# Performance work log

Hardware: AMD Instinct MI355X
Metric: run time of the kernel (lower is better)

The kernel has to match this reference:

```python
import jax, jax.numpy as jnp
import numpy as np

SOC, EOS = 3, 2
NUM_HEADS = 12
LN_EPS = 1e-5


def setup_inputs() -> dict:
    key = jax.random.key(0)
    ks = jax.random.split(key, 24)
    B, S, D, N, FF, K = 8, 4096, 768, 1024, 3072, 640
    img = jax.random.normal(ks[0], (B, N, D), jnp.float32)
    hid = jax.random.normal(ks[1], (B, S, D), jnp.float32)
    seq = jax.random.randint(ks[2], (B, S), 4, 100)
    m = jax.random.uniform(ks[3], (B, S)) < 0.125
    seq = jnp.where(m, SOC, seq).at[:, 0].set(SOC)  # ensure >=1 SOC per row
    w = lambda k, a, b: jax.random.normal(k, (a, b), jnp.float32) * 0.02
    return {
        "img": img, "hid": hid, "seq": seq,
        "wq_s": w(ks[4], D, D), "wk_s": w(ks[5], D, D), "wv_s": w(ks[6], D, D), "wo_s": w(ks[7], D, D),
        "wq_c": w(ks[8], D, D), "wk_c": w(ks[9], D, D), "wv_c": w(ks[10], D, D), "wo_c": w(ks[11], D, D),
        "w_ff1": w(ks[12], D, FF), "w_ff2": w(ks[13], FF, D),
        "ln1_s": jnp.ones((D,)), "ln1_b": jnp.zeros((D,)),
        "ln2_s": jnp.ones((D,)), "ln2_b": jnp.zeros((D,)),
        "ln3_s": jnp.ones((D,)), "ln3_b": jnp.zeros((D,)),
        "cap": K,
    }


def _ln(x, s, b):
    mu = jnp.mean(x, axis=-1, keepdims=True)
    var = jnp.var(x, axis=-1, keepdims=True)
    return (x - mu) * jax.lax.rsqrt(var + LN_EPS) * s + b


def _mha(q_in, kv_in, wq, wk, wv, wo, key_mask):
    # q_in [B,Lq,D], kv_in [B,Lk,D], key_mask [B,Lk] bool or None
    B, Lq, D = q_in.shape
    H = NUM_HEADS
    dh = D // H
    q = (q_in @ wq).reshape(B, Lq, H, dh)
    k = (kv_in @ wk).reshape(B, -1, H, dh)
    v = (kv_in @ wv).reshape(B, -1, H, dh)
    scores = jnp.einsum("bqhd,bkhd->bhqk", q, k) / np.sqrt(dh).astype(q.dtype)
    if key_mask is not None:
        scores = jnp.where(key_mask[:, None, None, :], scores, jnp.asarray(-1e9, scores.dtype))
    att = jax.nn.softmax(scores, axis=-1)
    out = jnp.einsum("bhqk,bkhd->bqhd", att, v).reshape(B, Lq, D)
    return out @ wo


def _extract(data, mask, cap):
    # data [B,S,...], mask [B,S] bool -> packed+zero-padded [B,cap,...]
    pos = jnp.cumsum(mask, axis=1) - 1          # slot for each valid token
    pos = jnp.where(mask, pos, cap)             # invalid tokens -> dump slot
    def one(d, p):
        buf = jnp.zeros((cap + 1,) + d.shape[1:], d.dtype)
        return buf.at[p].set(d)[:cap]
        # note: dump slot cap is sliced away
    return jax.vmap(one)(data, pos), pos


def reference(img, hid, seq, wq_s, wk_s, wv_s, wo_s, wq_c, wk_c, wv_c, wo_c,
              w_ff1, w_ff2, ln1_s, ln1_b, ln2_s, ln2_b, ln3_s, ln3_b, cap):
    # mask: SOC tokens occurring before the first EOS
    soc = (seq == SOC) & (jnp.cumsum(seq == EOS, axis=1) == 0)  # [B,S]
    ext, pos = _extract(hid, soc, cap)                          # [B,K,D]
    counts = jnp.sum(soc, axis=1)                               # [B]
    run = jnp.arange(cap)[None, :] < counts[:, None]            # [B,K] valid slots

    # Blocks: pre-LN self-attn (key mask = run), cross-attn to img, FFN
    x = ext
    x = x + _mha(_ln(x, ln1_s, ln1_b), _ln(x, ln1_s, ln1_b), wq_s, wk_s, wv_s, wo_s, run)
    x = x + _mha(_ln(x, ln2_s, ln2_b), img, wq_c, wk_c, wv_c, wo_c, None)
    h = _ln(x, ln3_s, ln3_b)
    x = x + jax.nn.gelu(h @ w_ff1) @ w_ff2

    # masked_scatter back: each SOC position (b,s) takes x[b, pos[b,s]]
    idx = jnp.clip(pos, 0, cap - 1)
    gathered = jnp.take_along_axis(x, idx[:, :, None], axis=1)  # [B,S,D]
    hid_new = jnp.where(soc[:, :, None], gathered, hid)
    return hid_new, x
```

## Files before the change

### kernel.cpp

```cpp
#include <hip/hip_runtime.h>
#include <hip/hip_bf16.h>


#define B_    8
#define S_    4096
#define D_    768
#define N_    1024
#define FF_   3072
#define H_    12
#define DH_   64
#define KCAP  640
#define SOC_TOK 3
#define EOS_TOK 2

typedef __hip_bfloat16 bf16;
typedef unsigned short u16;
typedef __attribute__((ext_vector_type(8))) short short8;
typedef __attribute__((ext_vector_type(4))) float f32x4;

__device__ __forceinline__ u16 ftou16(float x){ union{bf16 b; u16 s;} c; c.b = __float2bfloat16(x); return c.s; }
__device__ __forceinline__ unsigned pk2(float lo, float hi){ return (unsigned)ftou16(lo) | ((unsigned)ftou16(hi)<<16); }

__device__ __forceinline__ f32x4 MFMA(short8 a, short8 b, f32x4 c){
  return __builtin_amdgcn_mfma_f32_16x16x32_bf16(a, b, c, 0, 0, 0);
}

__device__ __forceinline__ void gld16(const void* gp, void* lp){
  __builtin_amdgcn_global_load_lds(
    reinterpret_cast<const __attribute__((address_space(1))) unsigned int*>((size_t)gp),
    reinterpret_cast<__attribute__((address_space(3))) unsigned int*>((size_t)lp),
    16, 0, 0);
}

template<int N> __device__ __forceinline__ void vwait(){
  asm volatile("s_waitcnt vmcnt(%0)" :: "i"(N) : "memory");
}
__device__ __forceinline__ void wgbar(){ asm volatile("s_barrier" ::: "memory"); }

__device__ __forceinline__ float fexp2(float x){ float r; asm("v_exp_f32 %0, %1" : "=v"(r) : "v"(x)); return r; }

__device__ __forceinline__ int xcd_swz(){
  int id = blockIdx.x;
  return (id & 7) * ((int)gridDim.x >> 3) + (id >> 3);
}

__device__ void scan_body(const int* __restrict__ seq, int* __restrict__ pos,
                          int* __restrict__ src, int* __restrict__ counts, int b){
  int tid = threadIdx.x;
  __shared__ int sd[256];
  __shared__ int carryE, carryS;
  if (tid==0){ carryE=0; carryS=0; }
  __syncthreads();
  for (int c=0; c<S_; c+=256){
    int s   = c + tid;
    int tok = seq[b*S_ + s];
    int isE = (tok==EOS_TOK) ? 1 : 0;
    int isS = (tok==SOC_TOK) ? 1 : 0;
    sd[tid]=isE; __syncthreads();
    for (int off=1; off<256; off<<=1){ int t_=(tid>=off)?sd[tid-off]:0; __syncthreads(); sd[tid]+=t_; __syncthreads(); }
    int eIncl = sd[tid];
    int eTot  = sd[255];
    int valid = (isS && (carryE + eIncl)==0) ? 1 : 0;
    __syncthreads();
    sd[tid]=valid; __syncthreads();
    for (int off=1; off<256; off<<=1){ int t_=(tid>=off)?sd[tid-off]:0; __syncthreads(); sd[tid]+=t_; __syncthreads(); }
    int vIncl = sd[tid];
    int vTot  = sd[255];
    if (valid){
      int slot = carryS + vIncl - 1;
      pos[b*S_ + s] = slot;
      if (slot < KCAP) src[b*KCAP + slot] = s;
    } else {
      pos[b*S_ + s] = -1;
    }
    __syncthreads();
    if (tid==0){ carryE += eTot; carryS += vTot; }
    __syncthreads();
  }
  if (tid==0) counts[b] = (carryS < KCAP) ? carryS : KCAP;
}

struct TransArgs { const float* w[10]; u16* o[10]; };
__global__ __launch_bounds__(256) void transpose_scan_k(TransArgs a, const int* __restrict__ seq,
                                                        int* __restrict__ pos, int* __restrict__ src,
                                                        int* __restrict__ counts,
                                                        const float* __restrict__ img, u16* __restrict__ imgB){
  int id = blockIdx.x;
  if (id >= 9224){
    int base = (id - 9224)*2048 + threadIdx.x*8;
    float4 a0 = *(const float4*)(img + base);
    float4 a1 = *(const float4*)(img + base + 4);
    uint4 wv;
    wv.x = pk2(a0.x,a0.y); wv.y = pk2(a0.z,a0.w); wv.z = pk2(a1.x,a1.y); wv.w = pk2(a1.z,a1.w);
    *(uint4*)(imgB + base) = wv;
    return;
  }
  if (id >= 9216){ scan_body(seq, pos, src, counts, id - 9216); return; }
  __shared__ float tile[32][33];
  int wi, t, K, N;
  if (id < 4608){ wi = id/576; t = id%576; K = 768; N = 768; }
  else if (id < 6912){ wi = 8; t = id-4608; K = 768; N = 3072; }
  else { wi = 9; t = id-6912; K = 3072; N = 768; }
  const float* in = a.w[wi]; u16* out = a.o[wi];
  int nbx = N >> 5;
  int bx = t % nbx, by = t / nbx;
  int tx = threadIdx.x & 31, ty = threadIdx.x >> 5;
  #pragma unroll
  for (int i=0;i<4;++i)
    tile[ty + i*8][tx] = in[(size_t)(by*32 + ty + i*8)*N + bx*32 + tx];
  __syncthreads();
  #pragma unroll
  for (int i=0;i<4;++i)
    out[(size_t)(bx*32 + ty + i*8)*K + by*32 + tx] = ftou16(tile[tx][ty + i*8]);
}

__global__ __launch_bounds__(256) void prep_k(const float* __restrict__ hid,
                                              const int* __restrict__ src,
                                              const int* __restrict__ counts,
                                              const int* __restrict__ pos,
                                              const float* __restrict__ g, const float* __restrict__ bt,
                                              float* __restrict__ X, u16* __restrict__ T0,
                                              float* __restrict__ out0){
  int id = blockIdx.x; int tid = threadIdx.x;
  if (id >= 5120){
    int base = (id - 5120)*4;
    #pragma unroll
    for (int r2=0;r2<4;++r2){
      int bs = base + r2;
      if (pos[bs] >= 0) continue;
      const float* hr = hid + (size_t)bs*D_;
      float* orow = out0 + (size_t)bs*D_;
      orow[tid]     = hr[tid];
      orow[tid+256] = hr[tid+256];
      orow[tid+512] = hr[tid+512];
    }
    return;
  }
  int bk = id; int b = bk / KCAP; int k = bk % KCAP;
  float v0, v1, v2;
  if (k < counts[b]){
    const float* hr = hid + ((size_t)b*S_ + src[b*KCAP + k])*D_;
    v0 = hr[tid]; v1 = hr[tid+256]; v2 = hr[tid+512];
  } else { v0 = v1 = v2 = 0.f; }
  float* xr = X + (size_t)bk*D_;
  xr[tid] = v0; xr[tid+256] = v1; xr[tid+512] = v2;
  float s1=v0+v1+v2, s2=v0*v0+v1*v1+v2*v2;
  for (int off=32; off; off>>=1){ s1+=__shfl_xor(s1,off); s2+=__shfl_xor(s2,off); }
  __shared__ float red[8];
  __shared__ float mu_s, rs_s;
  int w=tid>>6, ln=tid&63;
  if (ln==0){ red[w]=s1; red[4+w]=s2; }
  __syncthreads();
  if (tid==0){
    float S1=red[0]+red[1]+red[2]+red[3];
    float S2=red[4]+red[5]+red[6]+red[7];
    float mu = S1*(1.f/D_);
    float var= S2*(1.f/D_) - mu*mu;
    mu_s=mu; rs_s=rsqrtf(var + 1e-5f);
  }
  __syncthreads();
  float mu=mu_s, rs=rs_s;
  u16* yr = T0 + (size_t)bk*D_;
  yr[tid]     = ftou16((v0-mu)*rs*g[tid]     + bt[tid]);
  yr[tid+256] = ftou16((v1-mu)*rs*g[tid+256] + bt[tid+256]);
  yr[tid+512] = ftou16((v2-mu)*rs*g[tid+512] + bt[tid+512]);
}

__global__ __launch_bounds__(256) void ln_k(const float* __restrict__ X, u16* __restrict__ Y,
                                            const float* __restrict__ g, const float* __restrict__ bt){
  int r = blockIdx.x; int tid = threadIdx.x;
  const float* xr = X + (size_t)r*D_;
  float v0=xr[tid], v1=xr[tid+256], v2=xr[tid+512];
  float s1=v0+v1+v2, s2=v0*v0+v1*v1+v2*v2;
  for (int off=32; off; off>>=1){ s1+=__shfl_xor(s1,off); s2+=__shfl_xor(s2,off); }
  __shared__ float red[8];
  __shared__ float mu_s, rs_s;
  int w=tid>>6, ln=tid&63;
  if (ln==0){ red[w]=s1; red[4+w]=s2; }
  __syncthreads();
  if (tid==0){
    float S1=red[0]+red[1]+red[2]+red[3];
    float S2=red[4]+red[5]+red[6]+red[7];
    float mu = S1*(1.f/D_);
    float var= S2*(1.f/D_) - mu*mu;
    mu_s=mu; rs_s=rsqrtf(var + 1e-5f);
  }
  __syncthreads();
  float mu=mu_s, rs=rs_s;
  u16* yr = Y + (size_t)r*D_;
  yr[tid]     = ftou16((v0-mu)*rs*g[tid]     + bt[tid]);
  yr[tid+256] = ftou16((v1-mu)*rs*g[tid+256] + bt[tid+256]);
  yr[tid+512] = ftou16((v2-mu)*rs*g[tid+512] + bt[tid+512]);
}

template<int MODE, int BM, typename TA>
__device__ __forceinline__ void gemm_body(char* ldsp, const TA* __restrict__ A, const u16* __restrict__ Bt,
                                          void* __restrict__ C0, void* __restrict__ C1, void* __restrict__ C2,
                                          int wgid, int N, int K){
  constexpr int MI   = BM/32;
  constexpr int NBUF = (BM==128) ? 2 : ((sizeof(TA)==4) ? 2 : 3);
  u16* As = (u16*)ldsp;
  u16* Bs = (u16*)(ldsp + NBUF*(BM*32)*2);
  int nbx = N >> 7;
  int bx = wgid % nbx, by = wgid / nbx;
  int tid = threadIdx.x;
  int w = tid>>6, l = tid&63, g = l>>4, c = l&15;
  int wr = w&1, wc = w>>1;
  f32x4 acc[MI][4] = {};
  float4 rg[4];
  const int NK = K/32;

  auto STAGEB = [&](int buf, int kt){
    #pragma unroll
    for (int p=0;p<2;++p){
      int row = w*32 + p*16 + (l>>2);
      int su  = (l&3) ^ ((row>>1)&3);
      gld16((const void*)(Bt + (size_t)(bx*128+row)*K + kt + su*8), (void*)&Bs[buf*128*32 + (w*32+p*16)*32]);
    }
  };
  auto STAGEA16 = [&](int buf, int kt){
    if constexpr (BM==128){
      #pragma unroll
      for (int p=0;p<2;++p){
        int row = w*32 + p*16 + (l>>2);
        int su  = (l&3) ^ ((row>>1)&3);
        gld16((const void*)((const u16*)A + (size_t)(by*BM+row)*K + kt + su*8), (void*)&As[buf*BM*32 + (w*32+p*16)*32]);
      }
    } else {
      int row = w*16 + (l>>2);
      int su  = (l&3) ^ ((row>>1)&3);
      gld16((const void*)((const u16*)A + (size_t)(by*BM+row)*K + kt + su*8), (void*)&As[buf*BM*32 + (w*16)*32]);
    }
  };
  auto LOADREG = [&](int kt){
    if constexpr (BM==128){
      const float* ap = (const float*)A + (size_t)(by*BM + (tid>>1))*K + kt + (tid&1)*16;
      rg[0]=*(const float4*)ap;     rg[1]=*(const float4*)(ap+4);
      rg[2]=*(const float4*)(ap+8); rg[3]=*(const float4*)(ap+12);
    } else {
      const float* ap = (const float*)A + (size_t)(by*BM + (tid>>2))*K + kt + (tid&3)*8;
      rg[0] = *(const float4*)ap; rg[1] = *(const float4*)(ap+4);
    }
  };
  auto WRITEA = [&](int buf){
    if constexpr (BM==128){
      int row = tid>>1, half = tid&1;
      uint4 w0,w1;
      w0.x=pk2(rg[0].x,rg[0].y); w0.y=pk2(rg[0].z,rg[0].w); w0.z=pk2(rg[1].x,rg[1].y); w0.w=pk2(rg[1].z,rg[1].w);
      w1.x=pk2(rg[2].x,rg[2].y); w1.y=pk2(rg[2].z,rg[2].w); w1.z=pk2(rg[3].x,rg[3].y); w1.w=pk2(rg[3].z,rg[3].w);
      int sw = (row>>1)&3;
      *(uint4*)&As[buf*BM*32 + row*32 + ((half*2  )^sw)*8] = w0;
      *(uint4*)&As[buf*BM*32 + row*32 + ((half*2+1)^sw)*8] = w1;
    } else {
      int row = tid>>2, unit = tid&3;
      uint4 wv;
      wv.x=pk2(rg[0].x,rg[0].y); wv.y=pk2(rg[0].z,rg[0].w); wv.z=pk2(rg[1].x,rg[1].y); wv.w=pk2(rg[1].z,rg[1].w);
      int sw = (row>>1)&3;
      *(uint4*)&As[buf*BM*32 + row*32 + (unit^sw)*8] = wv;
    }
  };
  auto COMPUTE = [&](int buf){
    short8 af[MI], bfr[4];
    #pragma unroll
    for (int mi=0;mi<MI;++mi){ int row = wr*(MI*16) + mi*16 + c; af[mi]  = *(const short8*)&As[buf*BM*32 + row*32 + (g^((row>>1)&3))*8]; }
    #pragma unroll
    for (int ni=0;ni<4;++ni){ int row = wc*64 + ni*16 + c;       bfr[ni] = *(const short8*)&Bs[buf*128*32 + row*32 + (g^((row>>1)&3))*8]; }
    #pragma unroll
    for (int mi=0;mi<MI;++mi)
      #pragma unroll
      for (int ni=0;ni<4;++ni) acc[mi][ni] = MFMA(af[mi], bfr[ni], acc[mi][ni]);
  };

  if constexpr (BM==128 || sizeof(TA)==4){
    if constexpr (sizeof(TA)==4){ LOADREG(0); STAGEB(0,0); WRITEA(0); }
    else { STAGEA16(0,0); STAGEB(0,0); }
    __syncthreads();
    int buf = 0;
    for (int t=0;t<NK;++t){
      int ktn = (t+1)*32;
      if constexpr (sizeof(TA)==4){
        if (t+1<NK){ LOADREG(ktn); STAGEB(buf^1, ktn); }
        COMPUTE(buf);
        if (t+1<NK) WRITEA(buf^1);
      } else {
        if (t+1<NK){ STAGEA16(buf^1, ktn); STAGEB(buf^1, ktn); }
        COMPUTE(buf);
      }
      __syncthreads();
      buf ^= 1;
    }
  } else {
    constexpr int LPS = 3;
    STAGEA16(0,0);  STAGEB(0,0);
    STAGEA16(1,32); STAGEB(1,32);
    vwait<LPS>();
    wgbar();
    int buf = 0;
    for (int t=0;t<NK;++t){
      if (t+2 < NK){
        int nb = buf+2; if (nb>=3) nb-=3;
        STAGEA16(nb,(t+2)*32); STAGEB(nb,(t+2)*32);
      }
      COMPUTE(buf);
      if (t < NK-2) vwait<LPS>(); else vwait<0>();
      wgbar();
      ++buf; if (buf==3) buf=0;
    }
  }

  int row0 = by*BM + wr*(MI*16), col0 = bx*128 + wc*64;
  #pragma unroll
  for (int mi=0;mi<MI;++mi)
    #pragma unroll
    for (int ni=0;ni<4;++ni){
      int rowb = row0 + mi*16 + g*4;
      int col  = col0 + ni*16 + c;
      if (MODE==4 && col >= 1536){
        int vv = col - 1536; int bb = rowb / KCAP; int key = rowb - bb*KCAP;
        ushort4 pk;
        pk.x = ftou16(acc[mi][ni][0]); pk.y = ftou16(acc[mi][ni][1]);
        pk.z = ftou16(acc[mi][ni][2]); pk.w = ftou16(acc[mi][ni][3]);
        *(ushort4*)&((u16*)C2)[((size_t)(bb*768 + vv))*KCAP + key] = pk;
      } else if (MODE==5 && col >= 768){
        int vv = col - 768; int bb = rowb >> 10; int key = rowb & 1023;
        ushort4 pk;
        pk.x = ftou16(acc[mi][ni][0]); pk.y = ftou16(acc[mi][ni][1]);
        pk.z = ftou16(acc[mi][ni][2]); pk.w = ftou16(acc[mi][ni][3]);
        *(ushort4*)&((u16*)C2)[((size_t)(bb*768 + vv))*1024 + key] = pk;
      } else {
        #pragma unroll
        for (int r=0;r<4;++r){
          int row = rowb + r;
          float v = acc[mi][ni][r];
          if (MODE==0){
            ((u16*)C0)[(size_t)row*N + col] = ftou16(v);
          } else if (MODE==1){
            ((float*)C0)[(size_t)row*N + col] += v;
          } else if (MODE==2){
            float z2 = 1.5957691216057308f*(v + 0.044715f*v*v*v);
            float e  = __expf(z2);
            float th = 1.f - 2.f/(e + 1.f);
            ((u16*)C0)[(size_t)row*N + col] = ftou16(0.5f*v*(1.f+th));
          } else if (MODE==6){
            size_t idx = (size_t)row*N + col;
            ((float*)C1)[idx] = ((const float*)C0)[idx] + v;
          } else if (MODE==4){
            if (col < 768)  ((u16*)C0)[(size_t)row*768 + col]       = ftou16(v);
            else            ((u16*)C1)[(size_t)row*768 + col - 768] = ftou16(v);
          } else {
            ((u16*)C0)[(size_t)row*768 + col] = ftou16(v);
          }
        }
      }
    }
}

template<int MODE, int BM, typename TA>
__global__ __launch_bounds__(256) void gemm_k(const TA* __restrict__ A, const u16* __restrict__ Bt,
                                              void* __restrict__ C0, void* __restrict__ C1, void* __restrict__ C2,
                                              int N, int K){
  constexpr int NBUF = (BM==128) ? 2 : ((sizeof(TA)==4) ? 2 : 3);
  __shared__ __align__(16) char pool[NBUF*(BM+128)*32*2];
  gemm_body<MODE,BM,TA>(pool, A, Bt, C0, C1, C2, xcd_swz(), N, K);
}

__global__ __launch_bounds__(256) void mega1_k(const u16* __restrict__ T0, const u16* __restrict__ wqkv_st,
                                               u16* __restrict__ Qb, u16* __restrict__ Kb, u16* __restrict__ VtS,
                                               const u16* __restrict__ imgB, const u16* __restrict__ wkv_ct,
                                               u16* __restrict__ KbC, u16* __restrict__ VtC){
  __shared__ __align__(16) char pool[2*(128+128)*32*2];
  int wgid = xcd_swz();
  if (wgid < 720) gemm_body<4,128,u16>(pool, T0,   wqkv_st, Qb,  Kb,      VtS, wgid,     2304, 768);
  else            gemm_body<5,128,u16>(pool, imgB, wkv_ct,  KbC, nullptr, VtC, wgid-720, 1536, 768);
}

template<int MASKED>
__global__ __launch_bounds__(256) void attn_k(const u16* __restrict__ Q, const u16* __restrict__ Kb,
                                              const u16* __restrict__ Vt, u16* __restrict__ O,
                                              const int* __restrict__ counts, int Lk){
  constexpr float C2E  = 0.18033688011112043f;
  constexpr float THR2 = 11.541560327111707f;
  __shared__ __align__(16) u16 Ks[3][64*64];
  __shared__ __align__(16) u16 Vs[3][64*64];
  __shared__ __align__(16) u16 P[4][16][72];
  int tid = threadIdx.x;
  int w = tid>>6, l = tid&63, g = l>>4, c = l&15;
  int wgid = xcd_swz();
  int qc = wgid % 5;
  int bh = wgid / 5;
  int h = bh % H_, b = bh / H_;
  int q0 = qc*128 + w*32;
  int cnt = MASKED ? counts[b] : Lk;
  int nt = (cnt + 63) >> 6;

  short8 qf[2][2];
  #pragma unroll
  for (int mi=0;mi<2;++mi){
    const u16* Qrow = Q + ((size_t)(b*KCAP + q0 + mi*16 + c))*D_ + h*DH_;
    qf[mi][0] = *(const short8*)(Qrow + g*8);
    qf[mi][1] = *(const short8*)(Qrow + 32 + g*8);
  }

  int srow8 = (l>>3);
  int sunit = l&7;
  auto STAGE = [&](int buf, int kb){
    #pragma unroll
    for (int p=0;p<2;++p){
      int r0 = w*16 + p*8;
      int rowK = r0 + srow8;
      int su = sunit ^ (rowK&7);
      gld16((const void*)(Kb + ((size_t)(b*Lk + kb + rowK))*D_ + h*DH_ + su*8), (void*)&Ks[buf][r0*64]);
      gld16((const void*)(Vt + ((size_t)(b*D_ + h*DH_ + rowK))*Lk + kb + su*8), (void*)&Vs[buf][r0*64]);
    }
  };

  f32x4 o[2][4] = {};
  float m_[2][4], lp[2][4] = {};
  #pragma unroll
  for (int mi=0;mi<2;++mi)
    #pragma unroll
    for (int r=0;r<4;++r) m_[mi][r] = -1e30f;

  STAGE(0, 0);
  if (nt > 1){ STAGE(1, 64); vwait<4>(); } else { vwait<0>(); }
  wgbar();
  int buf = 0;
  for (int t=0; t<nt; ++t){
    int kb = t*64;
    if (t+2 < nt){
      int nb = buf+2; if (nb>=3) nb-=3;
      STAGE(nb, kb+128);
    }
    short8 fr[4][2];
    #pragma unroll
    for (int nb=0;nb<4;++nb)
      #pragma unroll
      for (int kh=0;kh<2;++kh)
        fr[nb][kh] = *(const short8*)&Ks[buf][(nb*16+c)*64 + (((kh<<2)|g) ^ (c&7))*8];
    float pv[2][4][4];
    #pragma unroll
    for (int mi=0;mi<2;++mi)
      #pragma unroll
      for (int nb=0;nb<4;++nb){
        f32x4 zz = {0.f,0.f,0.f,0.f};
        zz = MFMA(qf[mi][0], fr[nb][0], zz);
        zz = MFMA(qf[mi][1], fr[nb][1], zz);
        bool msk = MASKED && (kb + nb*16 + c >= cnt);
        #pragma unroll
        for (int r=0;r<4;++r) pv[mi][nb][r] = msk ? -1e30f : zz[r]*C2E;
      }
    float tm[2][4];
    bool need = false;
    #pragma unroll
    for (int mi=0;mi<2;++mi)
      #pragma unroll
      for (int r=0;r<4;++r){
        float v = fmaxf(fmaxf(pv[mi][0][r],pv[mi][1][r]), fmaxf(pv[mi][2][r],pv[mi][3][r]));
        v = fmaxf(v, __shfl_xor(v,1)); v = fmaxf(v, __shfl_xor(v,2));
        v = fmaxf(v, __shfl_xor(v,4)); v = fmaxf(v, __shfl_xor(v,8));
        tm[mi][r] = v;
        need = need || (v > m_[mi][r] + THR2);
      }
    if (__any(need)){
      #pragma unroll
      for (int mi=0;mi<2;++mi)
        #pragma unroll
        for (int r=0;r<4;++r){
          float nm = fmaxf(m_[mi][r], tm[mi][r]);
          float scl = fexp2(m_[mi][r] - nm);
          m_[mi][r] = nm;
          lp[mi][r] *= scl;
          #pragma unroll
          for (int nbd=0;nbd<4;++nbd) o[mi][nbd][r] *= scl;
        }
    }
    #pragma unroll
    for (int mi=0;mi<2;++mi)
      #pragma unroll
      for (int r=0;r<4;++r){
        float acc2 = lp[mi][r];
        #pragma unroll
        for (int nb=0;nb<4;++nb){
          float e = fexp2(pv[mi][nb][r] - m_[mi][r]);
          pv[mi][nb][r] = e; acc2 += e;
        }
        lp[mi][r] = acc2;
      }
    short8 fv[4][2];
    #pragma unroll
    for (int nbd=0;nbd<4;++nbd)
      #pragma unroll
      for (int kh=0;kh<2;++kh)
        fv[nbd][kh] = *(const short8*)&Vs[buf][(nbd*16+c)*64 + (((kh<<2)|g) ^ (c&7))*8];
    #pragma unroll
    for (int mi=0;mi<2;++mi){
      #pragma unroll
      for (int nb=0;nb<4;++nb)
        #pragma unroll
        for (int r=0;r<4;++r) P[w][g*4+r][nb*16+c] = ftou16(pv[mi][nb][r]);
      short8 pa0 = *(const short8*)&P[w][c][g*8];
      short8 pa1 = *(const short8*)&P[w][c][32 + g*8];
      #pragma unroll
      for (int nbd=0;nbd<4;++nbd){
        o[mi][nbd] = MFMA(pa0, fv[nbd][0], o[mi][nbd]);
        o[mi][nbd] = MFMA(pa1, fv[nbd][1], o[mi][nbd]);
      }
    }
    if (t < nt-2) vwait<4>(); else vwait<0>();
    wgbar();
    ++buf; if (buf==3) buf=0;
  }
  float linv[2][4];
  #pragma unroll
  for (int mi=0;mi<2;++mi)
    #pragma unroll
    for (int r=0;r<4;++r){
      float lf = lp[mi][r];
      lf += __shfl_xor(lf,1); lf += __shfl_xor(lf,2);
      lf += __shfl_xor(lf,4); lf += __shfl_xor(lf,8);
      linv[mi][r] = 1.f/lf;
    }
  #pragma unroll
  for (int mi=0;mi<2;++mi)
    #pragma unroll
    for (int nbd=0;nbd<4;++nbd)
      #pragma unroll
      for (int r=0;r<4;++r)
        O[((size_t)(b*KCAP + q0 + mi*16 + g*4 + r))*D_ + h*DH_ + nbd*16 + c] = ftou16(o[mi][nbd][r] * linv[mi][r]);
}

__global__ __launch_bounds__(256) void scatter_soc_k(const int* __restrict__ pos,
                                                     const float* __restrict__ out1,
                                                     float* __restrict__ out0){
  int base = blockIdx.x*4; int tid = threadIdx.x;
  #pragma unroll
  for (int r2=0;r2<4;++r2){
    int bs = base + r2;
    int p = pos[bs];
    if (p < 0) continue;
    int pc = p < KCAP ? p : (KCAP-1);
    int b = bs >> 12;
    const float* xr = out1 + ((size_t)(b*KCAP + pc))*D_;
    float* orow = out0 + (size_t)bs*D_;
    orow[tid]     = xr[tid];
    orow[tid+256] = xr[tid+256];
    orow[tid+512] = xr[tid+512];
  }
}

extern "C" void kernel_launch(void* const* d_in, const int* in_sizes, int n_in,
                              void* d_out, int out_size, void* d_ws, size_t ws_size,
                              hipStream_t stream){
  const float* img  = (const float*)d_in[0];
  const float* hid  = (const float*)d_in[1];
  const int*   seq  = (const int*)  d_in[2];
  const float* W[10] = { (const float*)d_in[3], (const float*)d_in[4], (const float*)d_in[5], (const float*)d_in[6],
                         (const float*)d_in[7], (const float*)d_in[8], (const float*)d_in[9], (const float*)d_in[10],
                         (const float*)d_in[11], (const float*)d_in[12] };
  const float* ln1s = (const float*)d_in[13];
  const float* ln1b = (const float*)d_in[14];
  const float* ln2s = (const float*)d_in[15];
  const float* ln2b = (const float*)d_in[16];
  const float* ln3s = (const float*)d_in[17];
  const float* ln3b = (const float*)d_in[18];

  char* ws = (char*)d_ws;
  int*   pos    = (int*)  (ws + 0);
  int*   src    = (int*)  (ws + 131072);
  int*   counts = (int*)  (ws + 151552);
  float* X      = (float*)(ws + 151808);
  u16*   T0     = (u16*)  (ws + 15880448);
  u16*   Qb     = (u16*)  (ws + 23744768);
  u16*   Kb     = (u16*)  (ws + 31609088);
  u16*   VtS    = (u16*)  (ws + 39473408);
  u16*   KbC    = (u16*)  (ws + 47337728);
  u16*   VtC    = (u16*)  (ws + 59920640);
  u16*   AO     = (u16*)  (ws + 72503552);
  u16*   Wt     = (u16*)  (ws + 80367872);
  u16*   MID    = Qb;

  u16* wqkv_st = Wt + 0ull*589824;
  u16* wo_st   = Wt + 3ull*589824;
  u16* wq_ct   = Wt + 4ull*589824;
  u16* wkv_ct  = Wt + 5ull*589824;
  u16* wo_ct   = Wt + 7ull*589824;
  u16* wff1t   = Wt + 8ull*589824;
  u16* wff2t   = wff1t + 2359296;

  float* out0 = (float*)d_out;
  float* out1 = out0 + (size_t)B_*S_*D_;
  u16* imgB = (u16*)out1;

  TransArgs ta;
  for (int i=0;i<10;++i) ta.w[i] = W[i];
  for (int i=0;i<8;++i)  ta.o[i] = Wt + (size_t)i*589824;
  ta.o[8] = wff1t; ta.o[9] = wff2t;

  transpose_scan_k<<<12296, 256, 0, stream>>>(ta, seq, pos, src, counts, img, imgB);
  prep_k<<<13312, 256, 0, stream>>>(hid, src, counts, pos, ln1s, ln1b, X, T0, out0);

  const int G_MEGA1 = 720 + 768;
  const int G_N768  = (5120/64)*(768/128);
  const int G_FF1   = (5120/128)*(3072/128);
  const int G_ATT   = B_*H_*5;

  mega1_k<<<G_MEGA1, 256, 0, stream>>>(T0, wqkv_st, Qb, Kb, VtS, imgB, wkv_ct, KbC, VtC);
  attn_k<1><<<G_ATT, 256, 0, stream>>>(Qb, Kb, VtS, AO, counts, KCAP);
  gemm_k<1,64,u16><<<G_N768, 256, 0, stream>>>(AO, wo_st, X, nullptr, nullptr, 768, 768);

  ln_k<<<5120, 256, 0, stream>>>(X, T0, ln2s, ln2b);
  gemm_k<0,64,u16><<<G_N768, 256, 0, stream>>>(T0, wq_ct, Qb, nullptr, nullptr, 768, 768);
  attn_k<0><<<G_ATT, 256, 0, stream>>>(Qb, KbC, VtC, AO, counts, N_);
  gemm_k<1,64,u16><<<G_N768, 256, 0, stream>>>(AO, wo_ct, X, nullptr, nullptr, 768, 768);

  ln_k<<<5120, 256, 0, stream>>>(X, T0, ln3s, ln3b);
  gemm_k<2,128,u16><<<G_FF1, 256, 0, stream>>>(T0, wff1t, MID, nullptr, nullptr, 3072, 768);
  gemm_k<6,64,u16><<<G_N768, 256, 0, stream>>>(MID, wff2t, X, out1, nullptr, 768, 3072);

  scatter_soc_k<<<8192, 256, 0, stream>>>(pos, out1, out0);
}
```

Before: 392.4 us.

## Use one wave per row in LayerNorm, exp2 GELU, and MFMA priority hints

LayerNorm now gives each row to a single 64-lane wave with float4 loads and packed bf16 stores, so the LDS reduction and the two block barriers go away and each launch has a quarter of the blocks. The GELU epilogue folds the 2·sqrt(2/π) scale into an exp2 constant. The attention kernel raises wave priority around its MFMA sections to favour matrix-core issue. Each change is small and affects a different kernel, and the fexp2 helper must already exist for this to compile.

```diff
diff --git a/kernel.cpp b/kernel.cpp
--- a/kernel.cpp
+++ b/kernel.cpp
@@ -168,29 +168,34 @@
 
 __global__ __launch_bounds__(256) void ln_k(const float* __restrict__ X, u16* __restrict__ Y,
                                             const float* __restrict__ g, const float* __restrict__ bt){
-  int r = blockIdx.x; int tid = threadIdx.x;
-  const float* xr = X + (size_t)r*D_;
-  float v0=xr[tid], v1=xr[tid+256], v2=xr[tid+512];
-  float s1=v0+v1+v2, s2=v0*v0+v1*v1+v2*v2;
+  int w = threadIdx.x>>6, l = threadIdx.x&63;
+  size_t r = (size_t)blockIdx.x*4 + w;
+  const float* xr = X + r*D_;
+  float4 v[3];
+  #pragma unroll
+  for (int i=0;i<3;++i) v[i] = *(const float4*)(xr + (l + 64*i)*4);
+  float s1=0.f, s2=0.f;
+  #pragma unroll
+  for (int i=0;i<3;++i){
+    s1 += v[i].x + v[i].y + v[i].z + v[i].w;
+    s2 += v[i].x*v[i].x + v[i].y*v[i].y + v[i].z*v[i].z + v[i].w*v[i].w;
+  }
+  #pragma unroll
   for (int off=32; off; off>>=1){ s1+=__shfl_xor(s1,off); s2+=__shfl_xor(s2,off); }
-  __shared__ float red[8];
-  __shared__ float mu_s, rs_s;
-  int w=tid>>6, ln=tid&63;
-  if (ln==0){ red[w]=s1; red[4+w]=s2; }
-  __syncthreads();
-  if (tid==0){
-    float S1=red[0]+red[1]+red[2]+red[3];
-    float S2=red[4]+red[5]+red[6]+red[7];
-    float mu = S1*(1.f/D_);
-    float var= S2*(1.f/D_) - mu*mu;
-    mu_s=mu; rs_s=rsqrtf(var + 1e-5f);
-  }
-  __syncthreads();
-  float mu=mu_s, rs=rs_s;
-  u16* yr = Y + (size_t)r*D_;
-  yr[tid]     = ftou16((v0-mu)*rs*g[tid]     + bt[tid]);
-  yr[tid+256] = ftou16((v1-mu)*rs*g[tid+256] + bt[tid+256]);
-  yr[tid+512] = ftou16((v2-mu)*rs*g[tid+512] + bt[tid+512]);
+  float mu = s1*(1.f/D_);
+  float rs = rsqrtf(s2*(1.f/D_) - mu*mu + 1e-5f);
+  u16* yr = Y + r*D_;
+  #pragma unroll
+  for (int i=0;i<3;++i){
+    float4 gv = *(const float4*)(g  + (l + 64*i)*4);
+    float4 bv = *(const float4*)(bt + (l + 64*i)*4);
+    ushort4 o;
+    o.x = ftou16((v[i].x-mu)*rs*gv.x + bv.x);
+    o.y = ftou16((v[i].y-mu)*rs*gv.y + bv.y);
+    o.z = ftou16((v[i].z-mu)*rs*gv.z + bv.z);
+    o.w = ftou16((v[i].w-mu)*rs*gv.w + bv.w);
+    *(ushort4*)(yr + (l + 64*i)*4) = o;
+  }
 }
 
 template<int MODE, int BM, typename TA>
@@ -337,8 +342,8 @@
           } else if (MODE==1){
             ((float*)C0)[(size_t)row*N + col] += v;
           } else if (MODE==2){
-            float z2 = 1.5957691216057308f*(v + 0.044715f*v*v*v);
-            float e  = __expf(z2);
+            float z = v + 0.044715f*v*v*v;
+            float e = fexp2(z * 2.3022082551f);
             float th = 1.f - 2.f/(e + 1.f);
             ((u16*)C0)[(size_t)row*N + col] = ftou16(0.5f*v*(1.f+th));
           } else if (MODE==6){
@@ -438,6 +443,7 @@
       for (int kh=0;kh<2;++kh)
         fr[nb][kh] = *(const short8*)&Ks[buf][(nb*16+c)*64 + (((kh<<2)|g) ^ (c&7))*8];
     float pv[2][4][4];
+    __builtin_amdgcn_s_setprio(1);
     #pragma unroll
     for (int mi=0;mi<2;++mi)
       #pragma unroll
@@ -449,6 +455,7 @@
         #pragma unroll
         for (int r=0;r<4;++r) pv[mi][nb][r] = msk ? -1e30f : zz[r]*C2E;
       }
+    __builtin_amdgcn_s_setprio(0);
     float tm[2][4];
     bool need = false;
     #pragma unroll
@@ -500,11 +507,13 @@
         for (int r=0;r<4;++r) P[w][g*4+r][nb*16+c] = ftou16(pv[mi][nb][r]);
       short8 pa0 = *(const short8*)&P[w][c][g*8];
       short8 pa1 = *(const short8*)&P[w][c][32 + g*8];
+      __builtin_amdgcn_s_setprio(1);
       #pragma unroll
       for (int nbd=0;nbd<4;++nbd){
         o[mi][nbd] = MFMA(pa0, fv[nbd][0], o[mi][nbd]);
         o[mi][nbd] = MFMA(pa1, fv[nbd][1], o[mi][nbd]);
       }
+      __builtin_amdgcn_s_setprio(0);
     }
     if (t < nt-2) vwait<4>(); else vwait<0>();
     wgbar();
@@ -603,17 +612,18 @@
   const int G_N768  = (5120/64)*(768/128);
   const int G_FF1   = (5120/128)*(3072/128);
   const int G_ATT   = B_*H_*5;
+  const int G_LN    = 5120/4;
 
   mega1_k<<<G_MEGA1, 256, 0, stream>>>(T0, wqkv_st, Qb, Kb, VtS, imgB, wkv_ct, KbC, VtC);
   attn_k<1><<<G_ATT, 256, 0, stream>>>(Qb, Kb, VtS, AO, counts, KCAP);
   gemm_k<1,64,u16><<<G_N768, 256, 0, stream>>>(AO, wo_st, X, nullptr, nullptr, 768, 768);
 
-  ln_k<<<5120, 256, 0, stream>>>(X, T0, ln2s, ln2b);
+  ln_k<<<G_LN, 256, 0, stream>>>(X, T0, ln2s, ln2b);
   gemm_k<0,64,u16><<<G_N768, 256, 0, stream>>>(T0, wq_ct, Qb, nullptr, nullptr, 768, 768);
   attn_k<0><<<G_ATT, 256, 0, stream>>>(Qb, KbC, VtC, AO, counts, N_);
   gemm_k<1,64,u16><<<G_N768, 256, 0, stream>>>(AO, wo_ct, X, nullptr, nullptr, 768, 768);
 
-  ln_k<<<5120, 256, 0, stream>>>(X, T0, ln3s, ln3b);
+  ln_k<<<G_LN, 256, 0, stream>>>(X, T0, ln3s, ln3b);
   gemm_k<2,128,u16><<<G_FF1, 256, 0, stream>>>(T0, wff1t, MID, nullptr, nullptr, 3072, 768);
   gemm_k<6,64,u16><<<G_N768, 256, 0, stream>>>(MID, wff2t, X, out1, nullptr, 768, 3072);
 
```

New measurement: 392.4 us. No clear change (-0.0%).
